# Optimization experiments

Hardware: AMD Instinct MI355X
Metric: run time of the kernel (lower is better)

The kernel has to match this reference:

```python
import jax, jax.numpy as jnp
import numpy as np

N_AGENTS = 32
UNIT_DIM = 32
STATE_DIM = 1200
N_HEAD = 8
EMBED = 64
KEY_HID = 2 * EMBED
HYPER = 256
V_HID = 4 * EMBED
ATTEND_REG_COEF = 0.001
BS, T = 128, 32


def setup_inputs() -> dict:
    key = jax.random.key(0)
    ks = jax.random.split(key, 12)
    def lin(k, shape, fan_in):
        return jax.random.normal(k, shape, jnp.float32) / np.sqrt(fan_in)
    return dict(
        agent_qs=jax.random.normal(ks[0], (BS, T, N_AGENTS), jnp.float32),
        states=jax.random.normal(ks[1], (BS, T, STATE_DIM), jnp.float32),
        actions=jax.random.randint(ks[2], (BS, T, N_AGENTS), 0, 20),
        sel_W1=lin(ks[3], (N_HEAD, HYPER, STATE_DIM), STATE_DIM),
        sel_b1=jnp.zeros((N_HEAD, HYPER), jnp.float32),
        sel_W2=lin(ks[4], (N_HEAD, EMBED, HYPER), HYPER),
        key_W1=lin(ks[5], (N_HEAD, KEY_HID, UNIT_DIM + 1), UNIT_DIM + 1),
        key_b1=jnp.zeros((N_HEAD, KEY_HID), jnp.float32),
        key_W2=lin(ks[6], (N_HEAD, EMBED, KEY_HID), KEY_HID),
        wh_W1=lin(ks[7], (HYPER, STATE_DIM), STATE_DIM),
        wh_b1=jnp.zeros((HYPER,), jnp.float32),
        wh_W2=lin(ks[8], (N_HEAD, HYPER), HYPER),
        wh_b2=jnp.zeros((N_HEAD,), jnp.float32),
        v_W1=lin(ks[9], (V_HID, STATE_DIM), STATE_DIM),
        v_b1=jnp.zeros((V_HID,), jnp.float32),
        v_W2=lin(ks[10], (1, V_HID), V_HID),
        v_b2=jnp.zeros((1,), jnp.float32),
    )


def reference(agent_qs, states, actions, sel_W1, sel_b1, sel_W2, key_W1, key_b1, key_W2,
              wh_W1, wh_b1, wh_W2, wh_b2, v_W1, v_b1, v_W2, v_b2):
    bs = agent_qs.shape[0]
    s = states.reshape(-1, STATE_DIM)                       # (B, S), B = bs*T
    B = s.shape[0]
    units = s[:, :UNIT_DIM * N_AGENTS].reshape(B, N_AGENTS, UNIT_DIM)  # (B, A, U)
    q = agent_qs.reshape(B, N_AGENTS)                       # (B, A)
    # nonlinear=True: append each agent's q to its unit features
    units = jnp.concatenate([units, q[:, :, None]], axis=2)  # (B, A, U+1)
    a = actions.reshape(B, N_AGENTS)
    # selector hypernets (all heads batched): (B, H, E)
    h1 = jax.nn.relu(jnp.einsum('bs,hes->bhe', s, sel_W1) + sel_b1[None])
    sel = jnp.einsum('bhe,hde->bhd', h1, sel_W2)
    # key hypernets (all heads x all agents batched): (B, H, A, E)
    k1 = jax.nn.relu(jnp.einsum('bau,hku->bhak', units, key_W1) + key_b1[None, :, None, :])
    keys = jnp.einsum('bhak,hdk->bhad', k1, key_W2)
    logits = jnp.einsum('bhd,bhad->bha', sel, keys)          # unscaled, used for regularizer
    scaled = logits / np.sqrt(EMBED)
    scaled = jnp.where(a[:, None, :] == 0, -99999999.0, scaled)  # mask_dead
    w = jax.nn.softmax(scaled, axis=2)                       # (B, H, A)
    head_q = jnp.einsum('ba,bha->bh', q, w)                  # (B, H)
    # weighted_head + state_bias
    wh = jnp.abs(jax.nn.relu(s @ wh_W1.T + wh_b1) @ wh_W2.T + wh_b2)  # (B, H)
    v = (jax.nn.relu(s @ v_W1.T + v_b1) @ v_W2.T + v_b2)[:, 0]        # (B,)
    y = (wh * head_q).sum(axis=1) + v
    q_tot = y.reshape(bs, -1, 1)
    # sum over heads of per-head mean of squared (unscaled) logits
    attend_mag_regs = ATTEND_REG_COEF * (logits ** 2).mean(axis=(0, 2)).sum()
    # per-head entropy: sum over agents, mean over batch
    head_entropies = -(jnp.log(w + 1e-8) * w).sum(axis=2).mean(axis=0)  # (H,)
    return q_tot, attend_mag_regs, head_entropies
```

## Files before the change

kernel.cpp:

```cpp
#include <hip/hip_runtime.h>

#define B_TOT 4096
#define SDIM  1200
#define KPAD  1216
#define NA    32
#define NH    8
#define EMB   64
#define KHID  128
#define HYP   256
#define NSEL  2048
#define NTOT  2560

#define WS_H1BF 0
#define WS_MBF  (WS_H1BF + (size_t)B_TOT * NTOT / 2)
#define WS_LG   (WS_MBF  + (size_t)B_TOT * NH * KHID / 2)
#define WS_PART (WS_LG   + (size_t)B_TOT * NH * NA)
#define WS_P2   (WS_PART + (size_t)B_TOT * 16)
#define WS_ABF  (WS_P2   + (size_t)32 * 16)
#define WS_WBF  (WS_ABF  + (size_t)B_TOT * KPAD / 2)
#define WS_KW32 (WS_WBF  + (size_t)NTOT * KPAD / 2)
#define WS_B2P  (WS_KW32 + (size_t)1024 * 32 / 2)
#define WS_M2T  (WS_B2P  + (size_t)2048 / 2)

#define CVT_A_BLK 4864
#define CVT_W_BLK 3040

typedef __attribute__((ext_vector_type(8))) short short8v;
typedef __attribute__((ext_vector_type(4))) float floatx4;

#define GLL16(gsrc, ldst) __builtin_amdgcn_global_load_lds( \
    (const __attribute__((address_space(1))) unsigned int*)(gsrc), \
    (__attribute__((address_space(3))) unsigned int*)(ldst), 16, 0, 0)

__device__ __forceinline__ ushort f2bf(float x) {
    unsigned u = __builtin_bit_cast(unsigned, x);
    unsigned r = (u + 0x7FFFu + ((u >> 16) & 1u)) >> 16;
    return (ushort)r;
}
__device__ __forceinline__ float bf2f(ushort u) {
    unsigned x = ((unsigned)u) << 16;
    return __builtin_bit_cast(float, x);
}

__global__ __launch_bounds__(256) void k_cvt_all(
    const float* __restrict__ states, const float* __restrict__ sel_W1,
    const float* __restrict__ wh_W1, const float* __restrict__ v_W1,
    const float* __restrict__ key_W1, const float* __restrict__ key_b1,
    ushort* __restrict__ Abf, ushort* __restrict__ Wbf,
    ushort* __restrict__ kw32, ushort* __restrict__ b2p)
{
    const int gb = blockIdx.x;
    if (gb < CVT_A_BLK) {
        const size_t g = (size_t)gb * 256 + threadIdx.x;
        const int row = (int)(g / (KPAD / 4));
        const int c4  = (int)(g % (KPAD / 4)) * 4;
        ushort4 o = {0, 0, 0, 0};
        if (c4 < SDIM) {
            float4 v = *(const float4*)(states + (size_t)row * SDIM + c4);
            o.x = f2bf(v.x); o.y = f2bf(v.y); o.z = f2bf(v.z); o.w = f2bf(v.w);
        }
        *(ushort4*)(Abf + (size_t)row * KPAD + c4) = o;
    } else if (gb < CVT_A_BLK + CVT_W_BLK) {
        const size_t g = (size_t)(gb - CVT_A_BLK) * 256 + threadIdx.x;
        const int row = (int)(g / (KPAD / 4));
        const int c4  = (int)(g % (KPAD / 4)) * 4;
        const float* src = (row < NSEL)       ? (sel_W1 + (size_t)row * SDIM)
                         : (row < NSEL + HYP) ? (wh_W1 + (size_t)(row - NSEL) * SDIM)
                                              : (v_W1  + (size_t)(row - NSEL - HYP) * SDIM);
        ushort4 o = {0, 0, 0, 0};
        if (c4 < SDIM) {
            float4 v = *(const float4*)(src + c4);
            o.x = f2bf(v.x); o.y = f2bf(v.y); o.z = f2bf(v.z); o.w = f2bf(v.w);
        }
        *(ushort4*)(Wbf + (size_t)row * KPAD + c4) = o;
    } else {
        const int row = (gb - CVT_A_BLK - CVT_W_BLK) * 256 + threadIdx.x;
        if (row >= 1024) return;
        const float* srcr = key_W1 + (size_t)row * 33;
        ushort o[32];
        #pragma unroll
        for (int u = 0; u < 32; ++u) o[u] = f2bf(srcr[u]);
        #pragma unroll
        for (int c = 0; c < 4; ++c)
            *(short8v*)(kw32 + (size_t)row * 32 + c * 8) = *(short8v*)&o[c * 8];
        const int h = row >> 7, k = row & 127;
        const size_t po = (((size_t)h * 16 + (k & 15)) * 8 + (k >> 4)) * 2;
        b2p[po]     = f2bf(srcr[32]);
        b2p[po + 1] = f2bf(key_b1[row]);
    }
}

__global__ __launch_bounds__(256) void k_m2(
    const float* __restrict__ sel_W2, const float* __restrict__ key_W2,
    ushort* __restrict__ M2T)
{
    __shared__ float ssel[EMB * HYP];
    __shared__ float skey[EMB][8];
    const int t  = threadIdx.x;
    const int h  = blockIdx.x;
    const int k0 = blockIdx.y * 8;

    const float4* sw = (const float4*)(sel_W2 + (size_t)h * EMB * HYP);
    #pragma unroll
    for (int j = 0; j < 16; ++j)
        ((float4*)ssel)[j * 256 + t] = sw[j * 256 + t];
    if (t < EMB) {
        #pragma unroll
        for (int kk = 0; kk < 8; ++kk)
            skey[t][kk] = key_W2[((size_t)h * EMB + t) * KHID + k0 + kk];
    }
    __syncthreads();

    const int e = t;
    float acc[8] = {};
    for (int d = 0; d < EMB; ++d) {
        const float sv = ssel[d * HYP + e];
        #pragma unroll
        for (int kk = 0; kk < 8; ++kk)
            acc[kk] = fmaf(sv, skey[d][kk], acc[kk]);
    }
    #pragma unroll
    for (int kk = 0; kk < 8; ++kk)
        M2T[((size_t)h * KHID + k0 + kk) * HYP + e] = f2bf(acc[kk]);
}

#define BKG 64
__global__ __launch_bounds__(256) void k_gemm1_mfma(
    const ushort* __restrict__ Abf, const ushort* __restrict__ Wbf,
    const float* __restrict__ sel_b1, const float* __restrict__ wh_b1,
    const float* __restrict__ v_b1, ushort* __restrict__ h1bf)
{
    __shared__ ushort As[128 * BKG];
    __shared__ ushort Bs[128 * BKG];
    const int tid = threadIdx.x;
    const int l   = tid & 63;
    const int w   = tid >> 6;
    const int wM  = w >> 1, wN = w & 1;
    const int arow0 = blockIdx.y * 128;
    const int nrow0 = blockIdx.x * 128;

    const int srow   = tid >> 3;
    const int schunk = tid & 7;
    const int scol   = (schunk ^ (srow & 7)) * 8;
    const ushort* gA = Abf + (size_t)(arow0 + srow) * KPAD + scol;
    const ushort* gB = Wbf + (size_t)(nrow0 + srow) * KPAD + scol;
    ushort* lA = &As[tid * 8];
    ushort* lB = &Bs[tid * 8];

    floatx4 acc[4][4] = {};

    for (int k0 = 0; k0 < KPAD; k0 += BKG) {
        #pragma unroll
        for (int c = 0; c < 4; ++c) {
            GLL16(gA + (size_t)(c * 32) * KPAD + k0, lA + c * 2048);
            GLL16(gB + (size_t)(c * 32) * KPAD + k0, lB + c * 2048);
        }
        __syncthreads();

        #pragma unroll
        for (int kk = 0; kk < 2; ++kk) {
            const int ch = kk * 4 + (l >> 4);
            short8v av[4], bv[4];
            #pragma unroll
            for (int mi = 0; mi < 4; ++mi) {
                const int row = wM * 64 + mi * 16 + (l & 15);
                av[mi] = *(const short8v*)&As[row * BKG + (ch ^ (row & 7)) * 8];
            }
            #pragma unroll
            for (int ni = 0; ni < 4; ++ni) {
                const int row = wN * 64 + ni * 16 + (l & 15);
                bv[ni] = *(const short8v*)&Bs[row * BKG + (ch ^ (row & 7)) * 8];
            }
            #pragma unroll
            for (int mi = 0; mi < 4; ++mi)
                #pragma unroll
                for (int ni = 0; ni < 4; ++ni)
                    acc[mi][ni] = __builtin_amdgcn_mfma_f32_16x16x32_bf16(
                        av[mi], bv[ni], acc[mi][ni], 0, 0, 0);
        }
        __syncthreads();
    }

    float bias_n[4];
    #pragma unroll
    for (int ni = 0; ni < 4; ++ni) {
        const int col = nrow0 + wN * 64 + ni * 16 + (l & 15);
        bias_n[ni] = (col < NSEL)       ? sel_b1[col]
                   : (col < NSEL + HYP) ? wh_b1[col - NSEL]
                                        : v_b1[col - NSEL - HYP];
    }
    #pragma unroll
    for (int mi = 0; mi < 4; ++mi) {
        const int row = arow0 + wM * 64 + mi * 16 + (l >> 4) * 4;
        #pragma unroll
        for (int ni = 0; ni < 4; ++ni) {
            const int col = nrow0 + wN * 64 + ni * 16 + (l & 15);
            #pragma unroll
            for (int r = 0; r < 4; ++r)
                h1bf[(size_t)(row + r) * NTOT + col] =
                    f2bf(fmaxf(acc[mi][ni][r] + bias_n[ni], 0.f));
        }
    }
}

#define BK 32
__global__ __launch_bounds__(256) void k_m_mfma(
    const ushort* __restrict__ h1bf, const ushort* __restrict__ M2T,
    ushort* __restrict__ m_out)
{
    __shared__ ushort As[2][64 * BK];
    __shared__ ushort Bs[2][128 * BK];
    const int tid = threadIdx.x;
    const int l   = tid & 63;
    const int w   = tid >> 6;
    const int wM  = w >> 1, wN = w & 1;
    const int h     = blockIdx.x;
    const int brow0 = blockIdx.y * 64;

    const int srow = tid >> 2;
    const int skof = (tid & 3) * 8;
    const ushort* gA = h1bf + (size_t)(brow0 + srow) * NTOT + h * HYP + skof;
    const ushort* gB = M2T + ((size_t)h * KHID + srow) * HYP + skof;

#define STAGE_M(BUF, KK) do { \
    GLL16(gA + (KK), &As[BUF][srow * BK + skof]); \
    GLL16(gB + (KK), &Bs[BUF][srow * BK + skof]); \
    GLL16(gB + (size_t)64 * HYP + (KK), &Bs[BUF][(64 + srow) * BK + skof]); \
} while (0)

    floatx4 acc[2][4] = {};

    STAGE_M(0, 0);
    __syncthreads();
    int cur = 0;
    for (int k0 = 0; k0 < HYP; k0 += BK) {
        if (k0 + BK < HYP) STAGE_M(cur ^ 1, k0 + BK);

        const int kch = (l >> 4) * 8;
        short8v av[2], bv[4];
        #pragma unroll
        for (int mi = 0; mi < 2; ++mi)
            av[mi] = *(const short8v*)&As[cur][(wM * 32 + mi * 16 + (l & 15)) * BK + kch];
        #pragma unroll
        for (int ni = 0; ni < 4; ++ni)
            bv[ni] = *(const short8v*)&Bs[cur][(wN * 64 + ni * 16 + (l & 15)) * BK + kch];
        #pragma unroll
        for (int mi = 0; mi < 2; ++mi)
            #pragma unroll
            for (int ni = 0; ni < 4; ++ni)
                acc[mi][ni] = __builtin_amdgcn_mfma_f32_16x16x32_bf16(
                    av[mi], bv[ni], acc[mi][ni], 0, 0, 0);
        __syncthreads();
        cur ^= 1;
    }

    #pragma unroll
    for (int mi = 0; mi < 2; ++mi) {
        const int row = brow0 + wM * 32 + mi * 16 + (l >> 4) * 4;
        #pragma unroll
        for (int ni = 0; ni < 4; ++ni) {
            const int col = wN * 64 + ni * 16 + (l & 15);
            #pragma unroll
            for (int r = 0; r < 4; ++r)
                m_out[(((size_t)(row + r) * NH + h) * 16 + (col & 15)) * 8 + (col >> 4)]
                    = f2bf(acc[mi][ni][r]);
        }
    }
}

__global__ __launch_bounds__(256) void k_logits_mfma(
    const ushort* __restrict__ Abf, const ushort* __restrict__ KW32,
    const ushort* __restrict__ B2p, const float* __restrict__ agent_qs,
    const ushort* __restrict__ mT, float* __restrict__ logits)
{
    const int tid = threadIdx.x;
    const int l   = tid & 63;
    const int w   = tid >> 6;
    const int b   = blockIdx.x * 4 + w;

    short8v av[2];
    float4 qv[2];
    #pragma unroll
    for (int mi = 0; mi < 2; ++mi) {
        const int a = mi * 16 + (l & 15);
        av[mi] = *(const short8v*)(
            Abf + (size_t)b * KPAD + a * 32 + (l >> 4) * 8);
        qv[mi] = *(const float4*)(
            agent_qs + (size_t)b * NA + mi * 16 + (l >> 4) * 4);
    }

    for (int h = 0; h < NH; ++h) {
        short8v bv[8];
        #pragma unroll
        for (int ni = 0; ni < 8; ++ni) {
            const int k = ni * 16 + (l & 15);
            bv[ni] = *(const short8v*)(
                KW32 + ((size_t)h * KHID + k) * 32 + (l >> 4) * 8);
        }
        const int bpo = (h * 16 + (l & 15)) * 16;
        short8v wb0 = *(const short8v*)&B2p[bpo];
        short8v wb1 = *(const short8v*)&B2p[bpo + 8];
        short8v mv = *(const short8v*)(
            mT + (((size_t)b * NH + h) * 16 + (l & 15)) * 8);
        float mr[8], w32r[8], b1r[8];
        #pragma unroll
        for (int ni = 0; ni < 8; ++ni) {
            mr[ni]   = bf2f((ushort)mv[ni]);
            w32r[ni] = bf2f((ushort)((ni < 4) ? wb0[ni * 2]     : wb1[(ni - 4) * 2]));
            b1r[ni]  = bf2f((ushort)((ni < 4) ? wb0[ni * 2 + 1] : wb1[(ni - 4) * 2 + 1]));
        }

        floatx4 acc[2][8] = {};
        #pragma unroll
        for (int mi = 0; mi < 2; ++mi)
            #pragma unroll
            for (int ni = 0; ni < 8; ++ni)
                acc[mi][ni] = __builtin_amdgcn_mfma_f32_16x16x32_bf16(
                    av[mi], bv[ni], acc[mi][ni], 0, 0, 0);

        #pragma unroll
        for (int mi = 0; mi < 2; ++mi) {
            float s0 = 0.f, s1 = 0.f, s2 = 0.f, s3 = 0.f;
            #pragma unroll
            for (int ni = 0; ni < 8; ++ni) {
                const float b1v = b1r[ni], wv = w32r[ni], mv2 = mr[ni];
                s0 = fmaf(fmaxf(fmaf(qv[mi].x, wv, acc[mi][ni][0] + b1v), 0.f), mv2, s0);
                s1 = fmaf(fmaxf(fmaf(qv[mi].y, wv, acc[mi][ni][1] + b1v), 0.f), mv2, s1);
                s2 = fmaf(fmaxf(fmaf(qv[mi].z, wv, acc[mi][ni][2] + b1v), 0.f), mv2, s2);
                s3 = fmaf(fmaxf(fmaf(qv[mi].w, wv, acc[mi][ni][3] + b1v), 0.f), mv2, s3);
            }
            #pragma unroll
            for (int off = 8; off >= 1; off >>= 1) {
                s0 += __shfl_xor(s0, off);
                s1 += __shfl_xor(s1, off);
                s2 += __shfl_xor(s2, off);
                s3 += __shfl_xor(s3, off);
            }
            if ((l & 15) == 0) {
                float4 o = {s0, s1, s2, s3};
                *(float4*)(logits + ((size_t)b * NH + h) * NA
                           + mi * 16 + (l >> 4) * 4) = o;
            }
        }
    }
}

__global__ __launch_bounds__(256) void k_softmax(
    const float* __restrict__ logits, const float* __restrict__ agent_qs,
    const int* __restrict__ actions, const ushort* __restrict__ h1bf,
    const float* __restrict__ wh_W2, const float* __restrict__ wh_b2,
    const float* __restrict__ v_W2, const float* __restrict__ v_b2,
    float* __restrict__ out, float* __restrict__ part)
{
    __shared__ float qs[NA];
    __shared__ int   act_s[NA];
    __shared__ float whs[NH];
    __shared__ float hq[NH];
    __shared__ float vred[4];
    const int b = blockIdx.x, t = threadIdx.x;
    if (t < NA) {
        qs[t]    = agent_qs[(size_t)b * NA + t];
        act_s[t] = actions[(size_t)b * NA + t];
    }
    const int h = t >> 5, a = t & 31;
    {
        float acc = 0.f;
        #pragma unroll
        for (int j = 0; j < 8; ++j) {
            const int e = a + 32 * j;
            acc = fmaf(bf2f(h1bf[(size_t)b * NTOT + NSEL + e]),
                       wh_W2[h * HYP + e], acc);
        }
        #pragma unroll
        for (int off = 16; off >= 1; off >>= 1) acc += __shfl_xor(acc, off, 32);
        if (a == 0) whs[h] = fabsf(acc + wh_b2[h]);
    }
    {
        float acc = bf2f(h1bf[(size_t)b * NTOT + NSEL + HYP + t]) * v_W2[t];
        #pragma unroll
        for (int off = 32; off >= 1; off >>= 1) acc += __shfl_xor(acc, off);
        if ((t & 63) == 0) vred[t >> 6] = acc;
    }
    __syncthreads();

    const float lg = logits[((size_t)b * NH + h) * NA + a];
    float sc = (act_s[a] == 0) ? -99999999.0f : lg * 0.125f;

    float mx = sc;
    #pragma unroll
    for (int off = 16; off >= 1; off >>= 1) mx = fmaxf(mx, __shfl_xor(mx, off, 32));
    const float e = expf(sc - mx);
    float sum = e;
    #pragma unroll
    for (int off = 16; off >= 1; off >>= 1) sum += __shfl_xor(sum, off, 32);
    const float wgt = e / sum;

    float r_sq  = lg * lg;
    float r_hq  = qs[a] * wgt;
    float r_ent = -wgt * logf(wgt + 1e-8f);
    #pragma unroll
    for (int off = 16; off >= 1; off >>= 1) {
        r_sq  += __shfl_xor(r_sq,  off, 32);
        r_hq  += __shfl_xor(r_hq,  off, 32);
        r_ent += __shfl_xor(r_ent, off, 32);
    }
    if (a == 0) {
        hq[h] = r_hq;
        part[(size_t)b * 16 + h]     = r_sq;
        part[(size_t)b * 16 + 8 + h] = r_ent;
    }
    __syncthreads();
    if (t == 0) {
        float y = vred[0] + vred[1] + vred[2] + vred[3] + v_b2[0];
        #pragma unroll
        for (int i = 0; i < NH; ++i) y = fmaf(whs[i], hq[i], y);
        out[b] = y;
    }
}

__global__ __launch_bounds__(256) void k_final_s1(
    const float* __restrict__ part, float* __restrict__ part2)
{
    __shared__ float red[16][17];
    const int t = threadIdx.x;
    const int c = t & 15, rl = t >> 4;
    const int rbase = blockIdx.x * 128 + rl;
    float v0 = 0.f, v1 = 0.f, v2 = 0.f, v3 = 0.f;
    #pragma unroll
    for (int j = 0; j < 8; j += 4) {
        v0 += part[(size_t)(rbase + (j + 0) * 16) * 16 + c];
        v1 += part[(size_t)(rbase + (j + 1) * 16) * 16 + c];
        v2 += part[(size_t)(rbase + (j + 2) * 16) * 16 + c];
        v3 += part[(size_t)(rbase + (j + 3) * 16) * 16 + c];
    }
    red[rl][c] = (v0 + v1) + (v2 + v3);
    __syncthreads();
    if (t < 16) {
        float s = 0.f;
        #pragma unroll
        for (int i = 0; i < 16; ++i) s += red[i][t];
        part2[blockIdx.x * 16 + t] = s;
    }
}

__global__ __launch_bounds__(256) void k_final_s2(
    const float* __restrict__ part2, float* __restrict__ out)
{
    __shared__ float red[16][17];
    __shared__ float tot[16];
    const int t = threadIdx.x;
    {
        const int g = t >> 4, c = t & 15;
        red[g][c] = part2[t] + part2[t + 256];
    }
    __syncthreads();
    if (t < 16) {
        float s = 0.f;
        #pragma unroll
        for (int i = 0; i < 16; ++i) s += red[i][t];
        tot[t] = s;
    }
    __syncthreads();
    if (t == 0) {
        float s = 0.f;
        #pragma unroll
        for (int i = 0; i < 8; ++i) s += tot[i];
        out[B_TOT] = 0.001f * (s / (float)((size_t)B_TOT * NA));
    }
    if (t >= 8 && t < 16)
        out[B_TOT + 1 + (t - 8)] = tot[t] / (float)B_TOT;
}

extern "C" void kernel_launch(void* const* d_in, const int* in_sizes, int n_in,
                              void* d_out, int out_size, void* d_ws, size_t ws_size,
                              hipStream_t stream) {
    (void)in_sizes; (void)n_in; (void)out_size; (void)ws_size;
    const float* agent_qs = (const float*)d_in[0];
    const float* states   = (const float*)d_in[1];
    const int*   actions  = (const int*)d_in[2];
    const float* sel_W1   = (const float*)d_in[3];
    const float* sel_b1   = (const float*)d_in[4];
    const float* sel_W2   = (const float*)d_in[5];
    const float* key_W1   = (const float*)d_in[6];
    const float* key_b1   = (const float*)d_in[7];
    const float* key_W2   = (const float*)d_in[8];
    const float* wh_W1    = (const float*)d_in[9];
    const float* wh_b1    = (const float*)d_in[10];
    const float* wh_W2    = (const float*)d_in[11];
    const float* wh_b2    = (const float*)d_in[12];
    const float* v_W1     = (const float*)d_in[13];
    const float* v_b1     = (const float*)d_in[14];
    const float* v_W2     = (const float*)d_in[15];
    const float* v_b2     = (const float*)d_in[16];

    float* out = (float*)d_out;
    float* ws  = (float*)d_ws;
    ushort* h1bf  = (ushort*)(ws + WS_H1BF);
    ushort* m_buf = (ushort*)(ws + WS_MBF);
    float* lg_buf = ws + WS_LG;
    float* part   = ws + WS_PART;
    float* part2  = ws + WS_P2;
    ushort* Abf   = (ushort*)(ws + WS_ABF);
    ushort* Wbf   = (ushort*)(ws + WS_WBF);
    ushort* KW32  = (ushort*)(ws + WS_KW32);
    ushort* B2p   = (ushort*)(ws + WS_B2P);
    ushort* M2T   = (ushort*)(ws + WS_M2T);

    k_cvt_all<<<CVT_A_BLK + CVT_W_BLK + 4, 256, 0, stream>>>(
        states, sel_W1, wh_W1, v_W1, key_W1, key_b1, Abf, Wbf, KW32, B2p);
    k_m2<<<dim3(NH, KHID / 8), 256, 0, stream>>>(sel_W2, key_W2, M2T);
    k_gemm1_mfma<<<dim3(NTOT / 128, B_TOT / 128), 256, 0, stream>>>(
        Abf, Wbf, sel_b1, wh_b1, v_b1, h1bf);
    k_m_mfma<<<dim3(NH, B_TOT / 64), 256, 0, stream>>>(h1bf, M2T, m_buf);
    k_logits_mfma<<<dim3(B_TOT / 4), 256, 0, stream>>>(
        Abf, KW32, B2p, agent_qs, m_buf, lg_buf);
    k_softmax<<<dim3(B_TOT), 256, 0, stream>>>(
        lg_buf, agent_qs, actions, h1bf, wh_W2, wh_b2, v_W2, v_b2, out, part);
    k_final_s1<<<32, 256, 0, stream>>>(part, part2);
    k_final_s2<<<1, 256, 0, stream>>>(part2, out);
}
```

Measured before the change: 109.4 us.

## Fuse softmax, entropy and mixing epilogue into the logits MFMA kernel

Moves the masked softmax, squared-logit and entropy partials, head-weight and state-bias computations into the logits kernel. Each wave now keeps its batch row's 8x32 logits in registers and reduces them with shuffles and a ballot-based dead mask. This removes the logits buffer round trip and one kernel launch of 4096 blocks. In exchange, each wave does per-head scalar reductions serially, which adds register pressure and latency to the MFMA kernel.

```diff
diff --git a/kernel.cpp b/kernel.cpp
--- a/kernel.cpp
+++ b/kernel.cpp
@@ -13,8 +13,7 @@
 
 #define WS_H1BF 0
 #define WS_MBF  (WS_H1BF + (size_t)B_TOT * NTOT / 2)
-#define WS_LG   (WS_MBF  + (size_t)B_TOT * NH * KHID / 2)
-#define WS_PART (WS_LG   + (size_t)B_TOT * NH * NA)
+#define WS_PART (WS_MBF  + (size_t)B_TOT * NH * KHID / 2)
 #define WS_P2   (WS_PART + (size_t)B_TOT * 16)
 #define WS_ABF  (WS_P2   + (size_t)32 * 16)
 #define WS_WBF  (WS_ABF  + (size_t)B_TOT * KPAD / 2)
@@ -268,10 +267,14 @@
     }
 }
 
-__global__ __launch_bounds__(256) void k_logits_mfma(
+__global__ __launch_bounds__(256) void k_logits_fused(
     const ushort* __restrict__ Abf, const ushort* __restrict__ KW32,
     const ushort* __restrict__ B2p, const float* __restrict__ agent_qs,
-    const ushort* __restrict__ mT, float* __restrict__ logits)
+    const ushort* __restrict__ mT, const int* __restrict__ actions,
+    const ushort* __restrict__ h1bf,
+    const float* __restrict__ wh_W2, const float* __restrict__ wh_b2,
+    const float* __restrict__ v_W2, const float* __restrict__ v_b2,
+    float* __restrict__ out, float* __restrict__ part)
 {
     const int tid = threadIdx.x;
     const int l   = tid & 63;
@@ -288,8 +291,33 @@
         qv[mi] = *(const float4*)(
             agent_qs + (size_t)b * NA + mi * 16 + (l >> 4) * 4);
     }
+    float qa[8] = {qv[0].x, qv[0].y, qv[0].z, qv[0].w,
+                   qv[1].x, qv[1].y, qv[1].z, qv[1].w};
+
+    const int actv = (l < NA) ? actions[(size_t)b * NA + l] : 1;
+    const unsigned dead = (unsigned)__ballot(actv == 0);
+
+    float vacc = 0.f;
+    float hwe[4];
+    #pragma unroll
+    for (int j = 0; j < 4; ++j) {
+        const int e = l + 64 * j;
+        vacc = fmaf(bf2f(h1bf[(size_t)b * NTOT + NSEL + HYP + e]), v_W2[e], vacc);
+        hwe[j] = bf2f(h1bf[(size_t)b * NTOT + NSEL + e]);
+    }
+    #pragma unroll
+    for (int off = 32; off >= 1; off >>= 1) vacc += __shfl_xor(vacc, off);
+    float y_acc = vacc + v_b2[0];
 
     for (int h = 0; h < NH; ++h) {
+        float wacc = 0.f;
+        #pragma unroll
+        for (int j = 0; j < 4; ++j)
+            wacc = fmaf(hwe[j], wh_W2[h * HYP + l + 64 * j], wacc);
+        #pragma unroll
+        for (int off = 32; off >= 1; off >>= 1) wacc += __shfl_xor(wacc, off);
+        const float wh_h = fabsf(wacc + wh_b2[h]);
+
         short8v bv[8];
         #pragma unroll
         for (int ni = 0; ni < 8; ++ni) {
@@ -318,16 +346,17 @@
                 acc[mi][ni] = __builtin_amdgcn_mfma_f32_16x16x32_bf16(
                     av[mi], bv[ni], acc[mi][ni], 0, 0, 0);
 
+        float lg8[8];
         #pragma unroll
         for (int mi = 0; mi < 2; ++mi) {
             float s0 = 0.f, s1 = 0.f, s2 = 0.f, s3 = 0.f;
             #pragma unroll
             for (int ni = 0; ni < 8; ++ni) {
                 const float b1v = b1r[ni], wv = w32r[ni], mv2 = mr[ni];
-                s0 = fmaf(fmaxf(fmaf(qv[mi].x, wv, acc[mi][ni][0] + b1v), 0.f), mv2, s0);
-                s1 = fmaf(fmaxf(fmaf(qv[mi].y, wv, acc[mi][ni][1] + b1v), 0.f), mv2, s1);
-                s2 = fmaf(fmaxf(fmaf(qv[mi].z, wv, acc[mi][ni][2] + b1v), 0.f), mv2, s2);
-                s3 = fmaf(fmaxf(fmaf(qv[mi].w, wv, acc[mi][ni][3] + b1v), 0.f), mv2, s3);
+                s0 = fmaf(fmaxf(fmaf(qa[mi * 4 + 0], wv, acc[mi][ni][0] + b1v), 0.f), mv2, s0);
+                s1 = fmaf(fmaxf(fmaf(qa[mi * 4 + 1], wv, acc[mi][ni][1] + b1v), 0.f), mv2, s1);
+                s2 = fmaf(fmaxf(fmaf(qa[mi * 4 + 2], wv, acc[mi][ni][2] + b1v), 0.f), mv2, s2);
+                s3 = fmaf(fmaxf(fmaf(qa[mi * 4 + 3], wv, acc[mi][ni][3] + b1v), 0.f), mv2, s3);
             }
             #pragma unroll
             for (int off = 8; off >= 1; off >>= 1) {
@@ -336,86 +365,46 @@
                 s2 += __shfl_xor(s2, off);
                 s3 += __shfl_xor(s3, off);
             }
-            if ((l & 15) == 0) {
-                float4 o = {s0, s1, s2, s3};
-                *(float4*)(logits + ((size_t)b * NH + h) * NA
-                           + mi * 16 + (l >> 4) * 4) = o;
-            }
-        }
-    }
-}
-
-__global__ __launch_bounds__(256) void k_softmax(
-    const float* __restrict__ logits, const float* __restrict__ agent_qs,
-    const int* __restrict__ actions, const ushort* __restrict__ h1bf,
-    const float* __restrict__ wh_W2, const float* __restrict__ wh_b2,
-    const float* __restrict__ v_W2, const float* __restrict__ v_b2,
-    float* __restrict__ out, float* __restrict__ part)
-{
-    __shared__ float qs[NA];
-    __shared__ int   act_s[NA];
-    __shared__ float whs[NH];
-    __shared__ float hq[NH];
-    __shared__ float vred[4];
-    const int b = blockIdx.x, t = threadIdx.x;
-    if (t < NA) {
-        qs[t]    = agent_qs[(size_t)b * NA + t];
-        act_s[t] = actions[(size_t)b * NA + t];
-    }
-    const int h = t >> 5, a = t & 31;
-    {
-        float acc = 0.f;
-        #pragma unroll
-        for (int j = 0; j < 8; ++j) {
-            const int e = a + 32 * j;
-            acc = fmaf(bf2f(h1bf[(size_t)b * NTOT + NSEL + e]),
-                       wh_W2[h * HYP + e], acc);
-        }
-        #pragma unroll
-        for (int off = 16; off >= 1; off >>= 1) acc += __shfl_xor(acc, off, 32);
-        if (a == 0) whs[h] = fabsf(acc + wh_b2[h]);
-    }
-    {
-        float acc = bf2f(h1bf[(size_t)b * NTOT + NSEL + HYP + t]) * v_W2[t];
-        #pragma unroll
-        for (int off = 32; off >= 1; off >>= 1) acc += __shfl_xor(acc, off);
-        if ((t & 63) == 0) vred[t >> 6] = acc;
-    }
-    __syncthreads();
-
-    const float lg = logits[((size_t)b * NH + h) * NA + a];
-    float sc = (act_s[a] == 0) ? -99999999.0f : lg * 0.125f;
-
-    float mx = sc;
-    #pragma unroll
-    for (int off = 16; off >= 1; off >>= 1) mx = fmaxf(mx, __shfl_xor(mx, off, 32));
-    const float e = expf(sc - mx);
-    float sum = e;
-    #pragma unroll
-    for (int off = 16; off >= 1; off >>= 1) sum += __shfl_xor(sum, off, 32);
-    const float wgt = e / sum;
-
-    float r_sq  = lg * lg;
-    float r_hq  = qs[a] * wgt;
-    float r_ent = -wgt * logf(wgt + 1e-8f);
-    #pragma unroll
-    for (int off = 16; off >= 1; off >>= 1) {
-        r_sq  += __shfl_xor(r_sq,  off, 32);
-        r_hq  += __shfl_xor(r_hq,  off, 32);
-        r_ent += __shfl_xor(r_ent, off, 32);
-    }
-    if (a == 0) {
-        hq[h] = r_hq;
-        part[(size_t)b * 16 + h]     = r_sq;
-        part[(size_t)b * 16 + 8 + h] = r_ent;
-    }
-    __syncthreads();
-    if (t == 0) {
-        float y = vred[0] + vred[1] + vred[2] + vred[3] + v_b2[0];
-        #pragma unroll
-        for (int i = 0; i < NH; ++i) y = fmaf(whs[i], hq[i], y);
-        out[b] = y;
-    }
+            lg8[mi * 4 + 0] = s0; lg8[mi * 4 + 1] = s1;
+            lg8[mi * 4 + 2] = s2; lg8[mi * 4 + 3] = s3;
+        }
+
+        const int abase = (l >> 4) * 4;
+        float sc[8], mx = -3.4e38f;
+        #pragma unroll
+        for (int i = 0; i < 8; ++i) {
+            const int a = (i >> 2) * 16 + abase + (i & 3);
+            sc[i] = ((dead >> a) & 1u) ? -99999999.0f : lg8[i] * 0.125f;
+            mx = fmaxf(mx, sc[i]);
+        }
+        mx = fmaxf(mx, __shfl_xor(mx, 16));
+        mx = fmaxf(mx, __shfl_xor(mx, 32));
+        float se = 0.f, r_sq = 0.f, ex[8];
+        #pragma unroll
+        for (int i = 0; i < 8; ++i) {
+            ex[i] = expf(sc[i] - mx);
+            se += ex[i];
+            r_sq = fmaf(lg8[i], lg8[i], r_sq);
+        }
+        se   += __shfl_xor(se, 16);   se   += __shfl_xor(se, 32);
+        r_sq += __shfl_xor(r_sq, 16); r_sq += __shfl_xor(r_sq, 32);
+        const float inv = 1.f / se;
+        float hq = 0.f, r_ent = 0.f;
+        #pragma unroll
+        for (int i = 0; i < 8; ++i) {
+            const float wgt = ex[i] * inv;
+            hq = fmaf(qa[i], wgt, hq);
+            r_ent -= wgt * logf(wgt + 1e-8f);
+        }
+        hq    += __shfl_xor(hq, 16);    hq    += __shfl_xor(hq, 32);
+        r_ent += __shfl_xor(r_ent, 16); r_ent += __shfl_xor(r_ent, 32);
+        y_acc = fmaf(wh_h, hq, y_acc);
+        if (l == 0) {
+            part[(size_t)b * 16 + h]     = r_sq;
+            part[(size_t)b * 16 + 8 + h] = r_ent;
+        }
+    }
+    if (l == 0) out[b] = y_acc;
 }
 
 __global__ __launch_bounds__(256) void k_final_s1(
@@ -497,7 +486,6 @@
     float* ws  = (float*)d_ws;
     ushort* h1bf  = (ushort*)(ws + WS_H1BF);
     ushort* m_buf = (ushort*)(ws + WS_MBF);
-    float* lg_buf = ws + WS_LG;
     float* part   = ws + WS_PART;
     float* part2  = ws + WS_P2;
     ushort* Abf   = (ushort*)(ws + WS_ABF);
@@ -512,10 +500,9 @@
     k_gemm1_mfma<<<dim3(NTOT / 128, B_TOT / 128), 256, 0, stream>>>(
         Abf, Wbf, sel_b1, wh_b1, v_b1, h1bf);
     k_m_mfma<<<dim3(NH, B_TOT / 64), 256, 0, stream>>>(h1bf, M2T, m_buf);
-    k_logits_mfma<<<dim3(B_TOT / 4), 256, 0, stream>>>(
-        Abf, KW32, B2p, agent_qs, m_buf, lg_buf);
-    k_softmax<<<dim3(B_TOT), 256, 0, stream>>>(
-        lg_buf, agent_qs, actions, h1bf, wh_W2, wh_b2, v_W2, v_b2, out, part);
+    k_logits_fused<<<dim3(B_TOT / 4), 256, 0, stream>>>(
+        Abf, KW32, B2p, agent_qs, m_buf, actions, h1bf,
+        wh_W2, wh_b2, v_W2, v_b2, out, part);
     k_final_s1<<<32, 256, 0, stream>>>(part, part2);
     k_final_s2<<<1, 256, 0, stream>>>(part2, out);
 }
```

Result: slower. 113.6 us (+3.9%).
